# Kernel tuning notes

Measured on AMD Instinct MI355X. Metric: run time of the kernel, lower is better.

## Reference

```python
import jax, jax.numpy as jnp
import numpy as np

EPS = 1e-20
K = 3  # kernel_size


def _patches(x, k=K):
    # emulates KernelChannels.kernel_channels / F.unfold with stride=1, padding=0, dilation=1
    # x: (B, C, H, W) -> (B, C, k*k, H-k+1, W-k+1); depth index kk = i*k + j maps to offset (i, j)
    Ho = x.shape[2] - k + 1
    Wo = x.shape[3] - k + 1
    return jnp.stack([x[:, :, i:i + Ho, j:j + Wo] for i in range(k) for j in range(k)], axis=2)


def setup_inputs() -> dict:
    key = jax.random.key(0)
    ks = jax.random.split(key, 13)
    B, C, O, H, W = 2, 32, 32, 256, 512
    Ho, Wo = H - K + 1, W - K + 1
    d = jax.random.uniform(ks[0], (B, C, H, W), dtype=jnp.float32)
    cd = jax.random.uniform(ks[1], (B, C, H, W), dtype=jnp.float32)
    s = jax.random.uniform(ks[2], (B, C, H, W), dtype=jnp.float32)
    cs = jax.random.uniform(ks[3], (B, C, H, W), dtype=jnp.float32)
    gx = jax.random.normal(ks[4], (B, C, H, W), dtype=jnp.float32)
    cgx = jax.random.uniform(ks[5], (B, C, H, W), dtype=jnp.float32)
    gy = jax.random.normal(ks[6], (B, C, H, W), dtype=jnp.float32)
    cgy = jax.random.uniform(ks[7], (B, C, H, W), dtype=jnp.float32)
    s_prod_roll = jax.random.uniform(ks[8], (B, C, K * K, Ho, Wo), dtype=jnp.float32)
    # learned parameters (raw; EnforcePos applies softplus inside forward)
    w_prop = jax.random.normal(ks[9], (1, 1, 1, 1), dtype=jnp.float32) * 0.1
    spatial_weight = jax.random.normal(ks[10], (C, 1, K * K, 1, 1), dtype=jnp.float32) * 0.1
    channel_weight = jax.random.normal(ks[11], (O, C, 1, 1), dtype=jnp.float32) * 0.1
    bias = jax.random.normal(ks[12], (1, O, 1, 1), dtype=jnp.float32) * 0.01
    return {"d": d, "cd": cd, "s": s, "cs": cs, "gx": gx, "cgx": cgx, "gy": gy,
            "cgy": cgy, "s_prod_roll": s_prod_roll, "w_prop": w_prop,
            "spatial_weight": spatial_weight, "channel_weight": channel_weight, "bias": bias}


def reference(d, cd, s, cs, gx, cgx, gy, cgy, s_prod_roll,
              w_prop, spatial_weight, channel_weight, bias):
    stride = 1
    # roll-based vertical neighbor gather with confidence zeroing at borders
    d_up = jnp.roll(d, 1, axis=2)
    cd_up = jnp.roll(cd, 1, axis=2).at[:, :, 0, :].set(0.0)
    s_up = jnp.roll(s, 1, axis=2)
    d_down = jnp.roll(d, -1, axis=2)
    cd_down = jnp.roll(cd, -1, axis=2).at[:, :, -1, :].set(0.0)
    s_down = jnp.roll(s, -1, axis=2)

    cgy_from_ds = s * s_up * s_down * cd_up * cd_up  # faithful to source (cd_up twice)
    height = (cd_up * d_up + cd_down * d_down) / (cd_up + cd_down + EPS)
    gy_from_ds = (d_down - d_up) / 2.0 / (height + EPS)

    w = jax.nn.softplus(w_prop)[0, 0, 0, 0]  # EnforcePos on w_prop
    gy_f = (w * cgy * gy + cgy_from_ds * gy_from_ds) / (w * cgy + cgy_from_ds + EPS)
    cgy_f = (w * cgy + cgy_from_ds) / (w + 1.0)

    # kernel-channel expansion (B, C, k*k, Ho, Wo)
    gy_roll = _patches(gy_f)
    cgy_roll = _patches(cgy_f)
    cgy_prop = cgy_roll * s_prod_roll

    # grouped conv3d with (C,1,k*k,1,1) kernel, groups=C == per-channel weighted sum over k*k
    sw = jax.nn.softplus(spatial_weight)[:, 0, :, 0, 0]  # (C, k*k)
    nom = jnp.einsum('bckhw,ck->bchw', cgy_prop * gy_roll, sw)
    den = jnp.einsum('bckhw,ck->bchw', cgy_prop, sw)
    gy_sp = nom / (den + EPS)
    cgy_sp = den / jnp.sum(sw)

    # 1x1 conv2d across channels (groups=1)
    cw = jax.nn.softplus(channel_weight)[:, :, 0, 0]  # (O, C)
    nom2 = jnp.einsum('bchw,oc->bohw', cgy_sp * gy_sp, cw)
    den2 = jnp.einsum('bchw,oc->bohw', cgy_sp, cw)
    gy_out = nom2 / (den2 + EPS) + bias
    cgy_out = den2 / jnp.sum(cw)
    return (gy_out * stride, cgy_out / stride / stride)
```

## Files before the change

### kernel.cpp

```cpp
#include <hip/hip_runtime.h>

#define EPSF 1e-20f

constexpr int B_ = 2, C_ = 32, O_ = 32, H_ = 256, W_ = 512;
constexpr int KS = 3;
constexpr int HO = H_ - KS + 1;
constexpr int WO = W_ - KS + 1;
constexpr int TH = 8;
constexpr int WT = 32;
constexpr long OUT1 = (long)B_ * O_ * HO * WO;

__device__ __forceinline__ float sp_(float x) { return log1pf(expf(x)); }

__global__ __launch_bounds__(256) void k_setup(const float* __restrict__ w_prop,
                                               const float* __restrict__ spw,
                                               const float* __restrict__ chw,
                                               float* __restrict__ params) {
  __shared__ float red[256];
  int t = threadIdx.x;
  float l1 = 0.f;
  for (int i = t; i < 288; i += 256) { float v = sp_(spw[i]); params[16 + i] = v; l1 += v; }
  red[t] = l1; __syncthreads();
  for (int k = 128; k > 0; k >>= 1) { if (t < k) red[t] += red[t + k]; __syncthreads(); }
  float SW = red[0]; __syncthreads();
  float l2 = 0.f;
  for (int i = t; i < 1024; i += 256) { float v = sp_(chw[i]); params[304 + i] = v; l2 += v; }
  red[t] = l2; __syncthreads();
  for (int k = 128; k > 0; k >>= 1) { if (t < k) red[t] += red[t + k]; __syncthreads(); }
  if (t == 0) { params[0] = sp_(w_prop[0]); params[1] = SW; params[2] = red[0]; }
}

__global__ __launch_bounds__(256) void k_fused(const float* __restrict__ d,
                                               const float* __restrict__ cd,
                                               const float* __restrict__ s,
                                               const float* __restrict__ gy,
                                               const float* __restrict__ cgy,
                                               const float* __restrict__ spr,
                                               const float* __restrict__ params,
                                               const float* __restrict__ bias,
                                               float* __restrict__ out) {
  __shared__ float gf[TH + 2][WT + 2];
  __shared__ float cf[TH + 2][WT + 2];
  __shared__ float sw_s[288];
  __shared__ float cw_s[1024];

  const int b   = blockIdx.z;
  const int ho0 = blockIdx.y * TH;
  const int wo0 = blockIdx.x * WT;
  const int t   = threadIdx.x;

  for (int i = t; i < 288; i += 256)  sw_s[i] = params[16 + i];
  for (int i = t; i < 1024; i += 256) cw_s[i] = params[304 + i];
  const float w      = params[0];
  const float inv_w1 = 1.0f / (w + 1.0f);
  const float invSW  = 1.0f / params[1];
  const float invCW  = 1.0f / params[2];

  const int tr = t >> 5;
  const int tw = t & 31;
  const int ho = ho0 + tr;
  const int wo = wo0 + tw;
  const bool valid = (ho < HO) && (wo < WO);

  float n2[O_], d2[O_];
#pragma unroll
  for (int o = 0; o < O_; ++o) { n2[o] = 0.f; d2[o] = 0.f; }

  constexpr int NPOS = (TH + 2) * (WT + 2);

  for (int c = 0; c < C_; ++c) {
    __syncthreads();
    const int cplane = (b * C_ + c) * H_ * W_;
    for (int pos = t; pos < NPOS; pos += 256) {
      const int r  = pos / (WT + 2);
      const int cc = pos - r * (WT + 2);
      const int gh = ho0 + r;
      const int gw = wo0 + cc;
      float vg = 0.f, vc = 0.f;
      if (gh < H_ && gw < W_) {
        const int base = cplane + gh * W_ + gw;
        const int up   = (gh == 0)      ? base + (H_ - 1) * W_ : base - W_;
        const int dn   = (gh == H_ - 1) ? base - (H_ - 1) * W_ : base + W_;
        const float cu  = (gh == 0)      ? 0.f : cd[up];
        const float cdn = (gh == H_ - 1) ? 0.f : cd[dn];
        const float du = d[up], dd = d[dn];
        const float cfd    = s[base] * s[up] * s[dn] * cu * cu;
        const float height = (cu * du + cdn * dd) / (cu + cdn + EPSF);
        const float gfd    = (dd - du) * 0.5f / (height + EPSF);
        const float a      = w * cgy[base];
        vg = (a * gy[base] + cfd * gfd) / (a + cfd + EPSF);
        vc = (a + cfd) * inv_w1;
      }
      (&gf[0][0])[pos] = vg;
      (&cf[0][0])[pos] = vc;
    }
    __syncthreads();

    if (valid) {
      const int sbase = (b * C_ + c) * 9 * (HO * WO) + ho * WO + wo;
      float nom = 0.f, den = 0.f;
#pragma unroll
      for (int i = 0; i < 3; ++i) {
#pragma unroll
        for (int j = 0; j < 3; ++j) {
          const float g   = gf[tr + i][tw + j];
          const float cg  = cf[tr + i][tw + j];
          const float spv = spr[sbase + (i * 3 + j) * (HO * WO)];
          const float swv = sw_s[c * 9 + i * 3 + j];
          const float cp  = cg * spv * swv;
          nom += cp * g;
          den += cp;
        }
      }
      const float gy_sp  = nom / (den + EPSF);
      const float cgy_sp = den * invSW;
      const float a      = gy_sp * cgy_sp;
#pragma unroll
      for (int o = 0; o < O_; ++o) {
        const float wv = cw_s[o * C_ + c];
        n2[o] += a * wv;
        d2[o] += cgy_sp * wv;
      }
    }
  }

  if (!valid) return;
#pragma unroll
  for (int o = 0; o < O_; ++o) {
    const int oidx = (b * O_ + o) * (HO * WO) + ho * WO + wo;
    out[oidx]        = n2[o] / (d2[o] + EPSF) + bias[o];
    out[OUT1 + oidx] = d2[o] * invCW;
  }
}

extern "C" void kernel_launch(void* const* d_in, const int* in_sizes, int n_in,
                              void* d_out, int out_size, void* d_ws, size_t ws_size,
                              hipStream_t stream) {
  const float* d      = (const float*)d_in[0];
  const float* cd     = (const float*)d_in[1];
  const float* s      = (const float*)d_in[2];
  const float* gy     = (const float*)d_in[6];
  const float* cgy    = (const float*)d_in[7];
  const float* spr    = (const float*)d_in[8];
  const float* w_prop = (const float*)d_in[9];
  const float* spw    = (const float*)d_in[10];
  const float* chw    = (const float*)d_in[11];
  const float* bias   = (const float*)d_in[12];
  float* out = (float*)d_out;

  float* params = (float*)d_ws;

  k_setup<<<1, 256, 0, stream>>>(w_prop, spw, chw, params);

  dim3 g((WO + WT - 1) / WT, (HO + TH - 1) / TH, B_);
  k_fused<<<g, 256, 0, stream>>>(d, cd, s, gy, cgy, spr, params, bias, out);
}
```

Baseline: 163.8 us.

## Replace shared-memory halo tiles with per-wavefront row segments using lane shuffles

```diff
diff --git a/kernel.cpp b/kernel.cpp
--- a/kernel.cpp
+++ b/kernel.cpp
@@ -3,11 +3,10 @@
 #define EPSF 1e-20f
 
 constexpr int B_ = 2, C_ = 32, O_ = 32, H_ = 256, W_ = 512;
-constexpr int KS = 3;
-constexpr int HO = H_ - KS + 1;
-constexpr int WO = W_ - KS + 1;
-constexpr int TH = 8;
-constexpr int WT = 32;
+constexpr int HO = 254, WO = 510;
+constexpr int SEG  = 62;
+constexpr int NSEG = (WO + SEG - 1) / SEG;
+constexpr int NWAVE = B_ * HO * NSEG;
 constexpr long OUT1 = (long)B_ * O_ * HO * WO;
 
 __device__ __forceinline__ float sp_(float x) { return log1pf(expf(x)); }
@@ -30,105 +29,108 @@
   if (t == 0) { params[0] = sp_(w_prop[0]); params[1] = SW; params[2] = red[0]; }
 }
 
-__global__ __launch_bounds__(256) void k_fused(const float* __restrict__ d,
-                                               const float* __restrict__ cd,
-                                               const float* __restrict__ s,
-                                               const float* __restrict__ gy,
-                                               const float* __restrict__ cgy,
-                                               const float* __restrict__ spr,
-                                               const float* __restrict__ params,
-                                               const float* __restrict__ bias,
-                                               float* __restrict__ out) {
-  __shared__ float gf[TH + 2][WT + 2];
-  __shared__ float cf[TH + 2][WT + 2];
+__global__ __launch_bounds__(256, 3) void k_fused(const float* __restrict__ d,
+                                                  const float* __restrict__ cd,
+                                                  const float* __restrict__ s,
+                                                  const float* __restrict__ gy,
+                                                  const float* __restrict__ cgy,
+                                                  const float* __restrict__ spr,
+                                                  const float* __restrict__ params,
+                                                  const float* __restrict__ bias,
+                                                  float* __restrict__ out) {
   __shared__ float sw_s[288];
   __shared__ float cw_s[1024];
+  __shared__ float bias_s[O_];
 
-  const int b   = blockIdx.z;
-  const int ho0 = blockIdx.y * TH;
-  const int wo0 = blockIdx.x * WT;
-  const int t   = threadIdx.x;
-
+  const int t = threadIdx.x;
   for (int i = t; i < 288; i += 256)  sw_s[i] = params[16 + i];
   for (int i = t; i < 1024; i += 256) cw_s[i] = params[304 + i];
+  if (t < O_) bias_s[t] = bias[t];
   const float w      = params[0];
   const float inv_w1 = 1.0f / (w + 1.0f);
   const float invSW  = 1.0f / params[1];
   const float invCW  = 1.0f / params[2];
+  __syncthreads();
 
-  const int tr = t >> 5;
-  const int tw = t & 31;
-  const int ho = ho0 + tr;
-  const int wo = wo0 + tw;
-  const bool valid = (ho < HO) && (wo < WO);
+  const int lane = t & 63;
+  const int wid  = blockIdx.x * 4 + (t >> 6);
+  if (wid >= NWAVE) return;
+  const int b    = wid / (HO * NSEG);
+  const int rem  = wid - b * (HO * NSEG);
+  const int ho   = rem / NSEG;
+  const int seg  = rem - ho * NSEG;
+  const int wo0  = seg * SEG;
+  const int wo   = wo0 + lane;
+  const int gw   = (wo < W_) ? wo : (W_ - 1);
+  const int wo_c = (wo < WO) ? wo : (WO - 1);
+  const bool valid = (lane < SEG) && (wo < WO);
 
   float n2[O_], d2[O_];
 #pragma unroll
   for (int o = 0; o < O_; ++o) { n2[o] = 0.f; d2[o] = 0.f; }
 
-  constexpr int NPOS = (TH + 2) * (WT + 2);
+  for (int c = 0; c < C_; ++c) {
+    const long cpl = (long)(b * C_ + c) * H_ * W_;
 
-  for (int c = 0; c < C_; ++c) {
-    __syncthreads();
-    const int cplane = (b * C_ + c) * H_ * W_;
-    for (int pos = t; pos < NPOS; pos += 256) {
-      const int r  = pos / (WT + 2);
-      const int cc = pos - r * (WT + 2);
-      const int gh = ho0 + r;
-      const int gw = wo0 + cc;
-      float vg = 0.f, vc = 0.f;
-      if (gh < H_ && gw < W_) {
-        const int base = cplane + gh * W_ + gw;
-        const int up   = (gh == 0)      ? base + (H_ - 1) * W_ : base - W_;
-        const int dn   = (gh == H_ - 1) ? base - (H_ - 1) * W_ : base + W_;
-        const float cu  = (gh == 0)      ? 0.f : cd[up];
-        const float cdn = (gh == H_ - 1) ? 0.f : cd[dn];
-        const float du = d[up], dd = d[dn];
-        const float cfd    = s[base] * s[up] * s[dn] * cu * cu;
-        const float height = (cu * du + cdn * dd) / (cu + cdn + EPSF);
-        const float gfd    = (dd - du) * 0.5f / (height + EPSF);
-        const float a      = w * cgy[base];
-        vg = (a * gy[base] + cfd * gfd) / (a + cfd + EPSF);
-        vc = (a + cfd) * inv_w1;
-      }
-      (&gf[0][0])[pos] = vg;
-      (&cf[0][0])[pos] = vc;
+    float dv[5], sv[5], cdv[5];
+#pragma unroll
+    for (int m = 0; m < 5; ++m) {
+      const int row = ho - 1 + m;
+      const int rw  = (row < 0) ? row + H_ : ((row >= H_) ? row - H_ : row);
+      const long a  = cpl + (long)rw * W_ + gw;
+      dv[m] = d[a];
+      sv[m] = s[a];
+      cdv[m] = (row < 0 || row >= H_) ? 0.f : cd[cpl + (long)row * W_ + gw];
     }
-    __syncthreads();
 
-    if (valid) {
-      const int sbase = (b * C_ + c) * 9 * (HO * WO) + ho * WO + wo;
-      float nom = 0.f, den = 0.f;
+    float gf[3], cf[3];
 #pragma unroll
-      for (int i = 0; i < 3; ++i) {
+    for (int r = 0; r < 3; ++r) {
+      const float cu  = cdv[r];
+      const float cdn = cdv[r + 2];
+      const float du  = dv[r], dd = dv[r + 2];
+      const long  ga  = cpl + (long)(ho + r) * W_ + gw;
+      const float cfd    = sv[r + 1] * sv[r] * sv[r + 2] * cu * cu;
+      const float height = (cu * du + cdn * dd) / (cu + cdn + EPSF);
+      const float gfd    = (dd - du) * 0.5f / (height + EPSF);
+      const float a      = w * cgy[ga];
+      gf[r] = (a * gy[ga] + cfd * gfd) / (a + cfd + EPSF);
+      cf[r] = (a + cfd) * inv_w1;
+    }
+
+    const long sbase = (long)(b * C_ + c) * 9 * (HO * WO) + (long)ho * WO + wo_c;
+    float nom = 0.f, den = 0.f;
 #pragma unroll
-        for (int j = 0; j < 3; ++j) {
-          const float g   = gf[tr + i][tw + j];
-          const float cg  = cf[tr + i][tw + j];
-          const float spv = spr[sbase + (i * 3 + j) * (HO * WO)];
-          const float swv = sw_s[c * 9 + i * 3 + j];
-          const float cp  = cg * spv * swv;
-          nom += cp * g;
-          den += cp;
-        }
-      }
-      const float gy_sp  = nom / (den + EPSF);
-      const float cgy_sp = den * invSW;
-      const float a      = gy_sp * cgy_sp;
+    for (int i = 0; i < 3; ++i) {
+      const float g0 = gf[i],              c0 = cf[i];
+      const float g1 = __shfl_down(g0, 1), c1 = __shfl_down(c0, 1);
+      const float g2 = __shfl_down(g0, 2), c2 = __shfl_down(c0, 2);
+      const float sp0 = spr[sbase + (long)(i * 3 + 0) * (HO * WO)];
+      const float sp1 = spr[sbase + (long)(i * 3 + 1) * (HO * WO)];
+      const float sp2 = spr[sbase + (long)(i * 3 + 2) * (HO * WO)];
+      const float cp0 = c0 * sp0 * sw_s[c * 9 + i * 3 + 0];
+      const float cp1 = c1 * sp1 * sw_s[c * 9 + i * 3 + 1];
+      const float cp2 = c2 * sp2 * sw_s[c * 9 + i * 3 + 2];
+      nom += cp0 * g0 + cp1 * g1 + cp2 * g2;
+      den += cp0 + cp1 + cp2;
+    }
+    const float gy_sp  = nom / (den + EPSF);
+    const float cgy_sp = den * invSW;
+    const float av     = gy_sp * cgy_sp;
+
 #pragma unroll
-      for (int o = 0; o < O_; ++o) {
-        const float wv = cw_s[o * C_ + c];
-        n2[o] += a * wv;
-        d2[o] += cgy_sp * wv;
-      }
+    for (int o = 0; o < O_; ++o) {
+      const float wv = cw_s[o * C_ + c];
+      n2[o] += av * wv;
+      d2[o] += cgy_sp * wv;
     }
   }
 
   if (!valid) return;
 #pragma unroll
   for (int o = 0; o < O_; ++o) {
-    const int oidx = (b * O_ + o) * (HO * WO) + ho * WO + wo;
-    out[oidx]        = n2[o] / (d2[o] + EPSF) + bias[o];
+    const long oidx = (long)(b * O_ + o) * (HO * WO) + (long)ho * WO + wo;
+    out[oidx]        = n2[o] / (d2[o] + EPSF) + bias_s[o];
     out[OUT1 + oidx] = d2[o] * invCW;
   }
 }
@@ -152,6 +154,6 @@
 
   k_setup<<<1, 256, 0, stream>>>(w_prop, spw, chw, params);
 
-  dim3 g((WO + WT - 1) / WT, (HO + TH - 1) / TH, B_);
-  k_fused<<<g, 256, 0, stream>>>(d, cd, s, gy, cgy, spr, params, bias, out);
+  const int nblk = (NWAVE + 3) / 4;
+  k_fused<<<nblk, 256, 0, stream>>>(d, cd, s, gy, cgy, spr, params, bias, out);
 }
```

After: 201.6 us. +23.0%, slower.

## Software-pipeline channel loads with double-buffered LDS tile and packed math

Applied to the files above, without the earlier changes.

```diff
diff --git a/kernel.cpp b/kernel.cpp
--- a/kernel.cpp
+++ b/kernel.cpp
@@ -2,15 +2,21 @@
 
 #define EPSF 1e-20f
 
+typedef float v2f __attribute__((ext_vector_type(2)));
+
 constexpr int B_ = 2, C_ = 32, O_ = 32, H_ = 256, W_ = 512;
-constexpr int KS = 3;
-constexpr int HO = H_ - KS + 1;
-constexpr int WO = W_ - KS + 1;
+constexpr int HO = 254, WO = 510;
 constexpr int TH = 8;
 constexpr int WT = 32;
-constexpr long OUT1 = (long)B_ * O_ * HO * WO;
+constexpr int TROW = TH + 2;
+constexpr int TCOL = WT + 2;
+constexpr int NPOS = TROW * TCOL;
+constexpr int HW  = H_ * W_;
+constexpr int PLO = HO * WO;
+constexpr int OUT1 = B_ * O_ * PLO;
 
 __device__ __forceinline__ float sp_(float x) { return log1pf(expf(x)); }
+__device__ __forceinline__ float rcp_(float x) { return __builtin_amdgcn_rcpf(x); }
 
 __global__ __launch_bounds__(256) void k_setup(const float* __restrict__ w_prop,
                                                const float* __restrict__ spw,
@@ -24,11 +30,18 @@
   for (int k = 128; k > 0; k >>= 1) { if (t < k) red[t] += red[t + k]; __syncthreads(); }
   float SW = red[0]; __syncthreads();
   float l2 = 0.f;
-  for (int i = t; i < 1024; i += 256) { float v = sp_(chw[i]); params[304 + i] = v; l2 += v; }
+  for (int i = t; i < 1024; i += 256) {
+    int o = i >> 5, c = i & 31;
+    float v = sp_(chw[o * C_ + c]);
+    params[304 + c * O_ + o] = v;
+    l2 += v;
+  }
   red[t] = l2; __syncthreads();
   for (int k = 128; k > 0; k >>= 1) { if (t < k) red[t] += red[t + k]; __syncthreads(); }
   if (t == 0) { params[0] = sp_(w_prop[0]); params[1] = SW; params[2] = red[0]; }
 }
+
+struct Raw { float du, dd, su, sb, sd, cu, cdn, gyv, cgyv; };
 
 __global__ __launch_bounds__(256) void k_fused(const float* __restrict__ d,
                                                const float* __restrict__ cd,
@@ -39,97 +52,131 @@
                                                const float* __restrict__ params,
                                                const float* __restrict__ bias,
                                                float* __restrict__ out) {
-  __shared__ float gf[TH + 2][WT + 2];
-  __shared__ float cf[TH + 2][WT + 2];
-  __shared__ float sw_s[288];
-  __shared__ float cw_s[1024];
+  __shared__ v2f tile[2][NPOS];
 
   const int b   = blockIdx.z;
   const int ho0 = blockIdx.y * TH;
   const int wo0 = blockIdx.x * WT;
   const int t   = threadIdx.x;
 
-  for (int i = t; i < 288; i += 256)  sw_s[i] = params[16 + i];
-  for (int i = t; i < 1024; i += 256) cw_s[i] = params[304 + i];
   const float w      = params[0];
-  const float inv_w1 = 1.0f / (w + 1.0f);
-  const float invSW  = 1.0f / params[1];
-  const float invCW  = 1.0f / params[2];
+  const float inv_w1 = rcp_(w + 1.0f);
+  const float invSW  = rcp_(params[1]);
+  const float invCW  = rcp_(params[2]);
+
+  const bool has1 = (t < NPOS - 256);
+  int bo[2], uo[2], doo[2];
+  float mu[2], md[2], pv[2];
+#pragma unroll
+  for (int sl = 0; sl < 2; ++sl) {
+    const int pos = t + sl * 256;
+    const int r  = pos / TCOL;
+    const int cc = pos - r * TCOL;
+    const int gh = ho0 + r;
+    const int gw = wo0 + cc;
+    const bool ok = (pos < NPOS) && (gh < H_) && (gw < W_);
+    const int ghc = ok ? gh : 0;
+    const int gwc = ok ? gw : 0;
+    const int base = ghc * W_ + gwc;
+    bo[sl]  = base;
+    uo[sl]  = (ghc == 0)      ? base + (H_ - 1) * W_ : base - W_;
+    doo[sl] = (ghc == H_ - 1) ? base - (H_ - 1) * W_ : base + W_;
+    mu[sl]  = (ghc == 0)      ? 0.f : 1.f;
+    md[sl]  = (ghc == H_ - 1) ? 0.f : 1.f;
+    pv[sl]  = ok ? 1.f : 0.f;
+  }
 
   const int tr = t >> 5;
   const int tw = t & 31;
   const int ho = ho0 + tr;
   const int wo = wo0 + tw;
   const bool valid = (ho < HO) && (wo < WO);
-
-  float n2[O_], d2[O_];
-#pragma unroll
-  for (int o = 0; o < O_; ++o) { n2[o] = 0.f; d2[o] = 0.f; }
-
-  constexpr int NPOS = (TH + 2) * (WT + 2);
+  const int ho_c = valid ? ho : 0;
+  const int wo_c = valid ? wo : 0;
+
+  const int cpl0   = b * C_ * HW;
+  const int sbase0 = b * C_ * 9 * PLO + ho_c * WO + wo_c;
+
+  auto load_raw = [&](int cpl, int sl, Raw& R) {
+    R.du   = d[cpl + uo[sl]];
+    R.dd   = d[cpl + doo[sl]];
+    R.su   = s[cpl + uo[sl]];
+    R.sb   = s[cpl + bo[sl]];
+    R.sd   = s[cpl + doo[sl]];
+    R.cu   = cd[cpl + uo[sl]];
+    R.cdn  = cd[cpl + doo[sl]];
+    R.gyv  = gy[cpl + bo[sl]];
+    R.cgyv = cgy[cpl + bo[sl]];
+  };
+
+  auto stage1 = [&](const Raw& R, int sl) -> v2f {
+    const float cu  = R.cu * mu[sl];
+    const float cdn = R.cdn * md[sl];
+    const float cfd = R.sb * R.su * R.sd * cu * cu;
+    const float height = (cu * R.du + cdn * R.dd) * rcp_(cu + cdn + EPSF);
+    const float gfd = (R.dd - R.du) * 0.5f * rcp_(height + EPSF);
+    const float a = w * R.cgyv;
+    const float vg = (a * R.gyv + cfd * gfd) * rcp_(a + cfd + EPSF);
+    const float vc = (a + cfd) * inv_w1;
+    return (v2f){vg * pv[sl], vc * pv[sl]};
+  };
+
+  Raw R0, R1;
+  float spn[9];
+  load_raw(cpl0, 0, R0);
+  if (has1) load_raw(cpl0, 1, R1);
+#pragma unroll
+  for (int k = 0; k < 9; ++k) spn[k] = spr[sbase0 + k * PLO];
+
+  v2f acc[O_];
+#pragma unroll
+  for (int o = 0; o < O_; ++o) acc[o] = (v2f){0.f, 0.f};
 
   for (int c = 0; c < C_; ++c) {
+    v2f* buf = tile[c & 1];
+    buf[t] = stage1(R0, 0);
+    if (has1) buf[t + 256] = stage1(R1, 1);
+
+    float spv[9];
+#pragma unroll
+    for (int k = 0; k < 9; ++k) spv[k] = spn[k];
+    const int cn = (c + 1 < C_) ? c + 1 : c;
+    const int cpl_n = cpl0 + cn * HW;
+    load_raw(cpl_n, 0, R0);
+    if (has1) load_raw(cpl_n, 1, R1);
+    const int sb_n = sbase0 + cn * 9 * PLO;
+#pragma unroll
+    for (int k = 0; k < 9; ++k) spn[k] = spr[sb_n + k * PLO];
+
     __syncthreads();
-    const int cplane = (b * C_ + c) * H_ * W_;
-    for (int pos = t; pos < NPOS; pos += 256) {
-      const int r  = pos / (WT + 2);
-      const int cc = pos - r * (WT + 2);
-      const int gh = ho0 + r;
-      const int gw = wo0 + cc;
-      float vg = 0.f, vc = 0.f;
-      if (gh < H_ && gw < W_) {
-        const int base = cplane + gh * W_ + gw;
-        const int up   = (gh == 0)      ? base + (H_ - 1) * W_ : base - W_;
-        const int dn   = (gh == H_ - 1) ? base - (H_ - 1) * W_ : base + W_;
-        const float cu  = (gh == 0)      ? 0.f : cd[up];
-        const float cdn = (gh == H_ - 1) ? 0.f : cd[dn];
-        const float du = d[up], dd = d[dn];
-        const float cfd    = s[base] * s[up] * s[dn] * cu * cu;
-        const float height = (cu * du + cdn * dd) / (cu + cdn + EPSF);
-        const float gfd    = (dd - du) * 0.5f / (height + EPSF);
-        const float a      = w * cgy[base];
-        vg = (a * gy[base] + cfd * gfd) / (a + cfd + EPSF);
-        vc = (a + cfd) * inv_w1;
-      }
-      (&gf[0][0])[pos] = vg;
-      (&cf[0][0])[pos] = vc;
-    }
-    __syncthreads();
-
-    if (valid) {
-      const int sbase = (b * C_ + c) * 9 * (HO * WO) + ho * WO + wo;
-      float nom = 0.f, den = 0.f;
-#pragma unroll
-      for (int i = 0; i < 3; ++i) {
-#pragma unroll
-        for (int j = 0; j < 3; ++j) {
-          const float g   = gf[tr + i][tw + j];
-          const float cg  = cf[tr + i][tw + j];
-          const float spv = spr[sbase + (i * 3 + j) * (HO * WO)];
-          const float swv = sw_s[c * 9 + i * 3 + j];
-          const float cp  = cg * spv * swv;
-          nom += cp * g;
-          den += cp;
-        }
-      }
-      const float gy_sp  = nom / (den + EPSF);
-      const float cgy_sp = den * invSW;
-      const float a      = gy_sp * cgy_sp;
-#pragma unroll
-      for (int o = 0; o < O_; ++o) {
-        const float wv = cw_s[o * C_ + c];
-        n2[o] += a * wv;
-        d2[o] += cgy_sp * wv;
+
+    const float* swc = params + 16 + c * 9;
+    float nom = 0.f, den = 0.f;
+#pragma unroll
+    for (int i = 0; i < 3; ++i) {
+#pragma unroll
+      for (int j = 0; j < 3; ++j) {
+        const v2f g = buf[(tr + i) * TCOL + tw + j];
+        const float cp = g.y * spv[i * 3 + j] * swc[i * 3 + j];
+        nom += cp * g.x;
+        den += cp;
       }
     }
+    const float gy_sp  = nom * rcp_(den + EPSF);
+    const float cgy_sp = den * invSW;
+    const v2f av2 = {gy_sp * cgy_sp, cgy_sp};
+
+    const float* cwc = params + 304 + c * O_;
+#pragma unroll
+    for (int o = 0; o < O_; ++o) acc[o] += av2 * cwc[o];
   }
 
   if (!valid) return;
+  const int obase = b * O_ * PLO + ho * WO + wo;
 #pragma unroll
   for (int o = 0; o < O_; ++o) {
-    const int oidx = (b * O_ + o) * (HO * WO) + ho * WO + wo;
-    out[oidx]        = n2[o] / (d2[o] + EPSF) + bias[o];
-    out[OUT1 + oidx] = d2[o] * invCW;
+    out[obase + o * PLO]        = acc[o].x / (acc[o].y + EPSF) + bias[o];
+    out[OUT1 + obase + o * PLO] = acc[o].y * invCW;
   }
 }
 
```

Measured after the change: 170.3 us. 3.9% more time.

## Split into precompute pass with bf16-packed intermediates and vectorized channel-mix kernel

Applied to the files above, without the earlier changes.

```diff
diff --git a/kernel.cpp b/kernel.cpp
--- a/kernel.cpp
+++ b/kernel.cpp
@@ -2,15 +2,28 @@
 
 #define EPSF 1e-20f
 
+typedef float v2f __attribute__((ext_vector_type(2)));
+
 constexpr int B_ = 2, C_ = 32, O_ = 32, H_ = 256, W_ = 512;
-constexpr int KS = 3;
-constexpr int HO = H_ - KS + 1;
-constexpr int WO = W_ - KS + 1;
-constexpr int TH = 8;
-constexpr int WT = 32;
-constexpr long OUT1 = (long)B_ * O_ * HO * WO;
+constexpr int HO = 254, WO = 510;
+constexpr int HW  = H_ * W_;
+constexpr int PLO = HO * WO;
+constexpr int OUT1 = B_ * O_ * PLO;
+constexpr int IMG  = B_ * C_ * HW;
+constexpr int WT2  = 64;
 
 __device__ __forceinline__ float sp_(float x) { return log1pf(expf(x)); }
+__device__ __forceinline__ float rcp_(float x) { return __builtin_amdgcn_rcpf(x); }
+
+__device__ __forceinline__ unsigned bfpack(float g, float c) {
+  unsigned ug = __float_as_uint(g);
+  unsigned uc = __float_as_uint(c);
+  ug = ug + 0x7FFFu + ((ug >> 16) & 1u);
+  uc = uc + 0x7FFFu + ((uc >> 16) & 1u);
+  return (ug >> 16) | (uc & 0xFFFF0000u);
+}
+__device__ __forceinline__ float bf_lo(unsigned u) { return __uint_as_float(u << 16); }
+__device__ __forceinline__ float bf_hi(unsigned u) { return __uint_as_float(u & 0xFFFF0000u); }
 
 __global__ __launch_bounds__(256) void k_setup(const float* __restrict__ w_prop,
                                                const float* __restrict__ spw,
@@ -24,112 +37,158 @@
   for (int k = 128; k > 0; k >>= 1) { if (t < k) red[t] += red[t + k]; __syncthreads(); }
   float SW = red[0]; __syncthreads();
   float l2 = 0.f;
-  for (int i = t; i < 1024; i += 256) { float v = sp_(chw[i]); params[304 + i] = v; l2 += v; }
+  for (int i = t; i < 1024; i += 256) {
+    int o = i >> 5, c = i & 31;
+    float v = sp_(chw[o * C_ + c]);
+    params[304 + c * O_ + o] = v;
+    l2 += v;
+  }
   red[t] = l2; __syncthreads();
   for (int k = 128; k > 0; k >>= 1) { if (t < k) red[t] += red[t + k]; __syncthreads(); }
   if (t == 0) { params[0] = sp_(w_prop[0]); params[1] = SW; params[2] = red[0]; }
 }
 
-__global__ __launch_bounds__(256) void k_fused(const float* __restrict__ d,
-                                               const float* __restrict__ cd,
-                                               const float* __restrict__ s,
-                                               const float* __restrict__ gy,
-                                               const float* __restrict__ cgy,
-                                               const float* __restrict__ spr,
-                                               const float* __restrict__ params,
-                                               const float* __restrict__ bias,
-                                               float* __restrict__ out) {
-  __shared__ float gf[TH + 2][WT + 2];
-  __shared__ float cf[TH + 2][WT + 2];
+__global__ __launch_bounds__(256) void k1_gyf(const float* __restrict__ d,
+                                              const float* __restrict__ cd,
+                                              const float* __restrict__ s,
+                                              const float* __restrict__ gy,
+                                              const float* __restrict__ cgy,
+                                              const float* __restrict__ params,
+                                              unsigned* __restrict__ I) {
+  const float w      = params[0];
+  const float inv_w1 = rcp_(w + 1.0f);
+  const int idx = blockIdx.x * 256 + threadIdx.x;
+  const long i4 = (long)idx * 4;
+  const int h = (int)((i4 >> 9) & (H_ - 1));
+  const long up = (h == 0)      ? i4 + (long)(H_ - 1) * W_ : i4 - W_;
+  const long dn = (h == H_ - 1) ? i4 - (long)(H_ - 1) * W_ : i4 + W_;
+
+  float4 duv = *(const float4*)(d + up);
+  float4 ddv = *(const float4*)(d + dn);
+  float4 sv  = *(const float4*)(s + i4);
+  float4 suv = *(const float4*)(s + up);
+  float4 sdv = *(const float4*)(s + dn);
+  float4 cduv = (h == 0)      ? make_float4(0.f, 0.f, 0.f, 0.f) : *(const float4*)(cd + up);
+  float4 cddv = (h == H_ - 1) ? make_float4(0.f, 0.f, 0.f, 0.f) : *(const float4*)(cd + dn);
+  float4 gyv  = *(const float4*)(gy + i4);
+  float4 cgyv = *(const float4*)(cgy + i4);
+
+  const float* pdu = (const float*)&duv;  const float* pdd = (const float*)&ddv;
+  const float* ps  = (const float*)&sv;   const float* psu = (const float*)&suv;
+  const float* psd = (const float*)&sdv;  const float* pcu = (const float*)&cduv;
+  const float* pcd = (const float*)&cddv; const float* pg  = (const float*)&gyv;
+  const float* pc  = (const float*)&cgyv;
+
+  uint4 o;
+  unsigned* po = (unsigned*)&o;
+#pragma unroll
+  for (int j = 0; j < 4; ++j) {
+    const float cu = pcu[j], cdn = pcd[j];
+    const float cfd = ps[j] * psu[j] * psd[j] * cu * cu;
+    const float height = (cu * pdu[j] + cdn * pdd[j]) * rcp_(cu + cdn + EPSF);
+    const float gfd = (pdd[j] - pdu[j]) * 0.5f * rcp_(height + EPSF);
+    const float a = w * pc[j];
+    const float vg = (a * pg[j] + cfd * gfd) * rcp_(a + cfd + EPSF);
+    const float vc = (a + cfd) * inv_w1;
+    po[j] = bfpack(vg, vc);
+  }
+  *(uint4*)(I + i4) = o;
+}
+
+__global__ __launch_bounds__(256) void k2_fused(const unsigned* __restrict__ I,
+                                                const float* __restrict__ spr,
+                                                const float* __restrict__ params,
+                                                const float* __restrict__ bias,
+                                                float* __restrict__ out) {
   __shared__ float sw_s[288];
-  __shared__ float cw_s[1024];
+  __shared__ v2f AB[C_][WT2 + 2];
 
   const int b   = blockIdx.z;
-  const int ho0 = blockIdx.y * TH;
-  const int wo0 = blockIdx.x * WT;
+  const int ho  = blockIdx.y;
+  const int wo0 = blockIdx.x * WT2;
   const int t   = threadIdx.x;
 
-  for (int i = t; i < 288; i += 256)  sw_s[i] = params[16 + i];
-  for (int i = t; i < 1024; i += 256) cw_s[i] = params[304 + i];
-  const float w      = params[0];
-  const float inv_w1 = 1.0f / (w + 1.0f);
-  const float invSW  = 1.0f / params[1];
-  const float invCW  = 1.0f / params[2];
-
-  const int tr = t >> 5;
-  const int tw = t & 31;
-  const int ho = ho0 + tr;
-  const int wo = wo0 + tw;
-  const bool valid = (ho < HO) && (wo < WO);
-
-  float n2[O_], d2[O_];
-#pragma unroll
-  for (int o = 0; o < O_; ++o) { n2[o] = 0.f; d2[o] = 0.f; }
-
-  constexpr int NPOS = (TH + 2) * (WT + 2);
-
-  for (int c = 0; c < C_; ++c) {
-    __syncthreads();
-    const int cplane = (b * C_ + c) * H_ * W_;
-    for (int pos = t; pos < NPOS; pos += 256) {
-      const int r  = pos / (WT + 2);
-      const int cc = pos - r * (WT + 2);
-      const int gh = ho0 + r;
-      const int gw = wo0 + cc;
-      float vg = 0.f, vc = 0.f;
-      if (gh < H_ && gw < W_) {
-        const int base = cplane + gh * W_ + gw;
-        const int up   = (gh == 0)      ? base + (H_ - 1) * W_ : base - W_;
-        const int dn   = (gh == H_ - 1) ? base - (H_ - 1) * W_ : base + W_;
-        const float cu  = (gh == 0)      ? 0.f : cd[up];
-        const float cdn = (gh == H_ - 1) ? 0.f : cd[dn];
-        const float du = d[up], dd = d[dn];
-        const float cfd    = s[base] * s[up] * s[dn] * cu * cu;
-        const float height = (cu * du + cdn * dd) / (cu + cdn + EPSF);
-        const float gfd    = (dd - du) * 0.5f / (height + EPSF);
-        const float a      = w * cgy[base];
-        vg = (a * gy[base] + cfd * gfd) / (a + cfd + EPSF);
-        vc = (a + cfd) * inv_w1;
-      }
-      (&gf[0][0])[pos] = vg;
-      (&cf[0][0])[pos] = vc;
-    }
-    __syncthreads();
-
-    if (valid) {
-      const int sbase = (b * C_ + c) * 9 * (HO * WO) + ho * WO + wo;
+  for (int i = t; i < 288; i += 256) sw_s[i] = params[16 + i];
+  const float invSW = rcp_(params[1]);
+  const float invCW = rcp_(params[2]);
+  __syncthreads();
+
+  const int pp = t & 31;
+  const int cg = t >> 5;
+  const int wo  = wo0 + 2 * pp;
+  const int wos = (wo <= WO - 2) ? wo : (WO - 2);
+
+#pragma unroll
+  for (int ci = 0; ci < 4; ++ci) {
+    const int c = cg * 4 + ci;
+    const unsigned* Ip = I + (b * C_ + c) * HW + ho * W_ + wos;
+    uint2 r0a = *(const uint2*)(Ip);
+    uint2 r0b = *(const uint2*)(Ip + 2);
+    uint2 r1a = *(const uint2*)(Ip + W_);
+    uint2 r1b = *(const uint2*)(Ip + W_ + 2);
+    uint2 r2a = *(const uint2*)(Ip + 2 * W_);
+    uint2 r2b = *(const uint2*)(Ip + 2 * W_ + 2);
+
+    const float* sp = spr + (long)(b * C_ + c) * 9 * PLO + ho * WO + wos;
+    v2f spv[9];
+#pragma unroll
+    for (int k = 0; k < 9; ++k) spv[k] = *(const v2f*)(sp + (long)k * PLO);
+
+    unsigned urow[3][4] = {{r0a.x, r0a.y, r0b.x, r0b.y},
+                           {r1a.x, r1a.y, r1b.x, r1b.y},
+                           {r2a.x, r2a.y, r2b.x, r2b.y}};
+    float gf[3][4], cf[3][4];
+#pragma unroll
+    for (int i = 0; i < 3; ++i)
+#pragma unroll
+      for (int j = 0; j < 4; ++j) { gf[i][j] = bf_lo(urow[i][j]); cf[i][j] = bf_hi(urow[i][j]); }
+
+#pragma unroll
+    for (int u = 0; u < 2; ++u) {
       float nom = 0.f, den = 0.f;
 #pragma unroll
       for (int i = 0; i < 3; ++i) {
 #pragma unroll
         for (int j = 0; j < 3; ++j) {
-          const float g   = gf[tr + i][tw + j];
-          const float cg  = cf[tr + i][tw + j];
-          const float spv = spr[sbase + (i * 3 + j) * (HO * WO)];
-          const float swv = sw_s[c * 9 + i * 3 + j];
-          const float cp  = cg * spv * swv;
-          nom += cp * g;
+          const float cp = cf[i][u + j] * spv[i * 3 + j][u] * sw_s[c * 9 + i * 3 + j];
+          nom += cp * gf[i][u + j];
           den += cp;
         }
       }
-      const float gy_sp  = nom / (den + EPSF);
+      const float gy_sp  = nom * rcp_(den + EPSF);
       const float cgy_sp = den * invSW;
-      const float a      = gy_sp * cgy_sp;
-#pragma unroll
-      for (int o = 0; o < O_; ++o) {
-        const float wv = cw_s[o * C_ + c];
-        n2[o] += a * wv;
-        d2[o] += cgy_sp * wv;
-      }
+      AB[c][2 * pp + u] = (v2f){gy_sp * cgy_sp, cgy_sp};
     }
   }
-
-  if (!valid) return;
-#pragma unroll
-  for (int o = 0; o < O_; ++o) {
-    const int oidx = (b * O_ + o) * (HO * WO) + ho * WO + wo;
-    out[oidx]        = n2[o] / (d2[o] + EPSF) + bias[o];
-    out[OUT1 + oidx] = d2[o] * invCW;
+  __syncthreads();
+
+  const int px  = t & 63;
+  const int og  = __builtin_amdgcn_readfirstlane(t >> 6);
+  const int wob = wo0 + px;
+
+  v2f ab[C_];
+#pragma unroll
+  for (int c = 0; c < C_; ++c) ab[c] = AB[c][px];
+
+  const float* cwT = params + 304;
+  v2f acc[8];
+#pragma unroll
+  for (int oj = 0; oj < 8; ++oj) acc[oj] = (v2f){0.f, 0.f};
+#pragma unroll
+  for (int c = 0; c < C_; ++c) {
+#pragma unroll
+    for (int oj = 0; oj < 8; ++oj)
+      acc[oj] += ab[c] * cwT[c * O_ + og * 8 + oj];
+  }
+
+  if (wob < WO) {
+    const int obase = b * O_ * PLO + ho * WO + wob;
+#pragma unroll
+    for (int oj = 0; oj < 8; ++oj) {
+      const int o = og * 8 + oj;
+      out[obase + o * PLO]        = acc[oj].x * rcp_(acc[oj].y + EPSF) + bias[o];
+      out[OUT1 + obase + o * PLO] = acc[oj].y * invCW;
+    }
   }
 }
 
@@ -149,9 +208,12 @@
   float* out = (float*)d_out;
 
   float* params = (float*)d_ws;
+  unsigned* I   = (unsigned*)d_ws + 4096;
 
   k_setup<<<1, 256, 0, stream>>>(w_prop, spw, chw, params);
 
-  dim3 g((WO + WT - 1) / WT, (HO + TH - 1) / TH, B_);
-  k_fused<<<g, 256, 0, stream>>>(d, cd, s, gy, cgy, spr, params, bias, out);
-}
+  k1_gyf<<<IMG / 4 / 256, 256, 0, stream>>>(d, cd, s, gy, cgy, params, I);
+
+  dim3 g2(8, HO, B_);
+  k2_fused<<<g2, 256, 0, stream>>>(I, spr, params, bias, out);
+}
```

After: 149.0 us. 1.1x faster.
